# Kernel optimization log

Measured on AMD Instinct MI355X. Metric: run time of the kernel, lower is better.

The kernel has to match this reference:

```python
import jax, jax.numpy as jnp
import numpy as np

DIM = 1024
NHEAD = 16
HEAD_DIM = DIM // NHEAD


def setup_inputs() -> dict:
    key = jax.random.key(0)
    k_x, k_wqkv, k_bqkv, k_wp, k_bp = jax.random.split(key, 5)
    scale = 1.0 / np.sqrt(DIM)
    return {
        "x": jax.random.normal(k_x, (4, 2048, DIM), dtype=jnp.float32),
        "w_qkv": jax.random.uniform(k_wqkv, (DIM, 3 * DIM), minval=-scale, maxval=scale, dtype=jnp.float32),
        "b_qkv": jax.random.uniform(k_bqkv, (3 * DIM,), minval=-scale, maxval=scale, dtype=jnp.float32),
        "w_proj": jax.random.uniform(k_wp, (DIM, DIM), minval=-scale, maxval=scale, dtype=jnp.float32),
        "b_proj": jax.random.uniform(k_bp, (DIM,), minval=-scale, maxval=scale, dtype=jnp.float32),
    }


def reference(x, w_qkv, b_qkv, w_proj, b_proj):
    B, N, D = x.shape
    # qkv projection: [B,N,3D] -> [3,B,H,N,hd]
    qkv = x @ w_qkv + b_qkv
    qkv = qkv.reshape(B, N, 3, NHEAD, HEAD_DIM).transpose(2, 0, 3, 1, 4)
    q, k, v = qkv[0], qkv[1], qkv[2]
    # naive full attention: scores [B,H,N,N]
    attn = jnp.einsum("bhqd,bhkd->bhqk", q, k) / jnp.sqrt(jnp.float32(HEAD_DIM))
    attn = jax.nn.softmax(attn, axis=-1)
    out = jnp.einsum("bhqk,bhkd->bhqd", attn, v)  # [B,H,N,hd]
    out = out.transpose(0, 2, 1, 3).reshape(B, N, D)
    return out @ w_proj + b_proj
```

## Files before the change

kernel.cpp:

```cpp
#include <hip/hip_runtime.h>
#include <math.h>

#define DIM     1024
#define NHEAD   16
#define HD      64
#define BATCH   4
#define SEQ     2048
#define MTOT    (BATCH * SEQ)
#define QKV_N   (3 * DIM)

typedef __attribute__((ext_vector_type(8))) short bf16x8;
typedef __attribute__((ext_vector_type(4))) float f32x4;
typedef unsigned int u32;
typedef unsigned short u16;

__device__ __forceinline__ u16 f2bf(float f) {
    u32 u = __float_as_uint(f);
    return (u16)((u + 0x7fffu + ((u >> 16) & 1u)) >> 16);
}

__device__ __forceinline__ float exp2_fast(float x) {
    float r; asm("v_exp_f32 %0, %1" : "=v"(r) : "v"(x)); return r;
}

__device__ __forceinline__ u32 cvtpk_bf16(float lo, float hi) {
    u32 r; asm("v_cvt_pk_bf16_f32 %0, %1, %2" : "=v"(r) : "v"(lo), "v"(hi));
    return r;
}

__device__ __forceinline__ void gload_lds16(const u16* g, u16* l) {
    __builtin_amdgcn_global_load_lds((const __attribute__((address_space(1))) u32*)g,
                                     (__attribute__((address_space(3))) u32*)l, 16, 0, 0);
}

__global__ __launch_bounds__(256) void cast_x(const float* __restrict__ in,
                                              u16* __restrict__ out) {
    const int i = (blockIdx.x * 256 + threadIdx.x) * 4;
    const float4 v = *(const float4*)&in[i];
    ushort4 o;
    o.x = f2bf(v.x); o.y = f2bf(v.y); o.z = f2bf(v.z); o.w = f2bf(v.w);
    *(ushort4*)&out[i] = o;
}

__global__ __launch_bounds__(256) void cast_transpose(const float* __restrict__ W,
                                                      u16* __restrict__ Wt,
                                                      int K, int N) {
    __shared__ float Ls[64][65];
    const int k0 = blockIdx.x * 64, n0 = blockIdx.y * 64;
    const int t = threadIdx.x;
    const int r = t >> 4, c4 = (t & 15) << 2;
    #pragma unroll
    for (int i = 0; i < 4; ++i) {
        const float4 v = *(const float4*)&W[(size_t)(k0 + r + i * 16) * N + n0 + c4];
        Ls[r + i * 16][c4 + 0] = v.x; Ls[r + i * 16][c4 + 1] = v.y;
        Ls[r + i * 16][c4 + 2] = v.z; Ls[r + i * 16][c4 + 3] = v.w;
    }
    __syncthreads();
    #pragma unroll
    for (int i = 0; i < 4; ++i) {
        const int nr = r + i * 16;
        ushort4 o;
        o.x = f2bf(Ls[c4 + 0][nr]); o.y = f2bf(Ls[c4 + 1][nr]);
        o.z = f2bf(Ls[c4 + 2][nr]); o.w = f2bf(Ls[c4 + 3][nr]);
        *(ushort4*)&Wt[(size_t)(n0 + nr) * K + k0 + c4] = o;
    }
}

#define GEMM_STAGE(buf, kof, Aptr, Bptr)                                       \
    _Pragma("unroll") for (int i = 0; i < 2; ++i) {                            \
        const int row = w * 32 + i * 16 + (lane >> 2);                         \
        const int slot = (lane & 3) ^ ((row >> 1) & 3);                        \
        gload_lds16(&Aptr[(size_t)(m0 + row) * DIM + (kof) + slot * 8],        \
                    &As[buf][(w * 32 + i * 16) * 32]);                         \
        gload_lds16(&Bptr[(size_t)(n0 + row) * DIM + (kof) + slot * 8],        \
                    &Bs[buf][(w * 32 + i * 16) * 32]);                         \
    }

#define GEMM_MAINLOOP(Aptr, Bptr)                                              \
    __shared__ __align__(16) u16 As[2][128 * 32];                              \
    __shared__ __align__(16) u16 Bs[2][128 * 32];                              \
    const int t = threadIdx.x;                                                 \
    const int lane = t & 63, w = t >> 6;                                       \
    const int n0 = blockIdx.x * 128;                                           \
    const int m0 = blockIdx.y * 128;                                           \
    const int wm = (w & 1) * 64, wn = (w >> 1) * 64;                           \
    const int g = lane >> 4, li = lane & 15;                                   \
    f32x4 acc[4][4];                                                           \
    _Pragma("unroll") for (int mt = 0; mt < 4; ++mt)                           \
        _Pragma("unroll") for (int nt = 0; nt < 4; ++nt)                       \
            acc[mt][nt] = (f32x4){0.f, 0.f, 0.f, 0.f};                         \
    GEMM_STAGE(0, 0, Aptr, Bptr)                                               \
    __syncthreads();                                                           \
    int cur = 0;                                                               \
    for (int k0 = 0; k0 < DIM; k0 += 32) {                                     \
        if (k0 + 32 < DIM) { GEMM_STAGE(cur ^ 1, k0 + 32, Aptr, Bptr) }        \
        bf16x8 a[4], b[4];                                                     \
        _Pragma("unroll") for (int mt = 0; mt < 4; ++mt) {                     \
            const int row = wm + mt * 16 + li;                                 \
            const int slot = g ^ ((row >> 1) & 3);                             \
            a[mt] = *(const bf16x8*)&As[cur][row * 32 + slot * 8];             \
        }                                                                      \
        _Pragma("unroll") for (int nt = 0; nt < 4; ++nt) {                     \
            const int row = wn + nt * 16 + li;                                 \
            const int slot = g ^ ((row >> 1) & 3);                             \
            b[nt] = *(const bf16x8*)&Bs[cur][row * 32 + slot * 8];             \
        }                                                                      \
        _Pragma("unroll") for (int mt = 0; mt < 4; ++mt)                       \
            _Pragma("unroll") for (int nt = 0; nt < 4; ++nt)                   \
                acc[mt][nt] = __builtin_amdgcn_mfma_f32_16x16x32_bf16(         \
                    a[mt], b[nt], acc[mt][nt], 0, 0, 0);                       \
        __syncthreads();                                                       \
        cur ^= 1;                                                              \
    }

#define QSCALE 0.18033688011112042f
__global__ __launch_bounds__(256) void gemm_qkv(
    const u16* __restrict__ A, const u16* __restrict__ Bt,
    const float* __restrict__ bias,
    u16* __restrict__ qo, u16* __restrict__ ko, u16* __restrict__ vo)
{
    GEMM_MAINLOOP(A, Bt)
    #pragma unroll
    for (int nt = 0; nt < 4; ++nt) {
        const int n = n0 + wn + nt * 16 + li;
        const int which = n >> 10;
        const int head  = (n >> 6) & 15;
        const int hd    = n & 63;
        const float bv = bias[n];
        if (which == 2) {
            #pragma unroll
            for (int mt = 0; mt < 4; ++mt) {
                const int m = m0 + wm + mt * 16 + g * 4;
                const int bb = m >> 11, tok = m & 2047;
                const u32 p0 = cvtpk_bf16(acc[mt][nt][0] + bv, acc[mt][nt][1] + bv);
                const u32 p1 = cvtpk_bf16(acc[mt][nt][2] + bv, acc[mt][nt][3] + bv);
                u16* d = &vo[((size_t)(bb * NHEAD + head) * HD + hd) * SEQ + tok];
                *(u32*)&d[0] = p0;
                *(u32*)&d[2] = p1;
            }
        } else {
            u16* dst = (which == 0) ? qo : ko;
            const float scale = (which == 0) ? QSCALE : 1.0f;
            #pragma unroll
            for (int mt = 0; mt < 4; ++mt) {
                #pragma unroll
                for (int r = 0; r < 4; ++r) {
                    const int m = m0 + wm + mt * 16 + g * 4 + r;
                    const int bb = m >> 11, tok = m & 2047;
                    dst[((size_t)(bb * NHEAD + head) * SEQ + tok) * HD + hd] =
                        f2bf((acc[mt][nt][r] + bv) * scale);
                }
            }
        }
    }
}

__global__ __launch_bounds__(256) void gemm_proj(
    const u16* __restrict__ A, const u16* __restrict__ Bt,
    const float* __restrict__ bias, float* __restrict__ out)
{
    GEMM_MAINLOOP(A, Bt)
    #pragma unroll
    for (int nt = 0; nt < 4; ++nt) {
        const int n = n0 + wn + nt * 16 + li;
        const float bv = bias[n];
        #pragma unroll
        for (int mt = 0; mt < 4; ++mt) {
            #pragma unroll
            for (int r = 0; r < 4; ++r) {
                const int m = m0 + wm + mt * 16 + g * 4 + r;
                out[(size_t)m * DIM + n] = acc[mt][nt][r] + bv;
            }
        }
    }
}

#define NKT  (SEQ / 64)
#define ATTN_STAGE(buf, ktile)                                                 \
    _Pragma("unroll") for (int i = 0; i < 2; ++i) {                            \
        const int rho = w * 16 + i * 8 + srow;                                 \
        const int key = (rho & 32) | (((rho >> 2) & 3) << 3)                   \
                      | (((rho >> 4) & 1) << 2) | (rho & 3);                   \
        const int sl = (sslot ^ (rho & 7)) << 3;                               \
        gload_lds16(&kg[(size_t)(ktile) * (64 * HD) + (size_t)key * HD + sl],  \
                    &Ks[buf][(w * 16 + i * 8) * 64]);                          \
        gload_lds16(&vg[(size_t)rho * SEQ + (ktile) * 64 + sl],                \
                    &Vs[buf][(w * 16 + i * 8) * 64]);                          \
    }

__global__ __launch_bounds__(256) void attn_mfma(
    const u16* __restrict__ q, const u16* __restrict__ k,
    const u16* __restrict__ v, u16* __restrict__ ao)
{
    __shared__ __align__(16) u16 Ks[2][64 * 64];
    __shared__ __align__(16) u16 Vs[2][64 * 64];

    const int t = threadIdx.x;
    const int lane = t & 63, w = t >> 6;
    const int g = lane >> 4, li = lane & 15;

    int flat = blockIdx.y * 16 + blockIdx.x;
    flat = (flat & 7) * 128 + (flat >> 3);
    const int q0 = (flat & 15) * 128;
    const int bh = flat >> 4;
    const size_t base = (size_t)bh * SEQ * HD;
    const u16* kg = k + base;
    const u16* vg = v + (size_t)bh * HD * SEQ;

    bf16x8 qf[2][2];
    #pragma unroll
    for (int h = 0; h < 2; ++h) {
        const size_t qrow = base + (size_t)(q0 + w * 32 + h * 16 + li) * HD;
        qf[h][0] = *(const bf16x8*)&q[qrow + g * 8];
        qf[h][1] = *(const bf16x8*)&q[qrow + 32 + g * 8];
    }

    float lsum[2] = {0.f, 0.f};
    f32x4 oacc[2][4];
    #pragma unroll
    for (int h = 0; h < 2; ++h)
        #pragma unroll
        for (int nt = 0; nt < 4; ++nt) oacc[h][nt] = (f32x4){0.f, 0.f, 0.f, 0.f};

    const int srow = lane >> 3;
    const int sslot = lane & 7;
    const int x8 = li & 7;

    ATTN_STAGE(0, 0)
    __syncthreads();

    int cur = 0;
    for (int kt = 0; kt < NKT; ++kt) {
        if (kt + 1 < NKT) { ATTN_STAGE(cur ^ 1, kt + 1) }
        const u16* Kc = Ks[cur];
        const u16* Vc = Vs[cur];

        f32x4 s[2][4];
        #pragma unroll
        for (int nt = 0; nt < 4; ++nt) {
            const int rowb = (nt * 16 + li) << 6;
            const bf16x8 kf0 = *(const bf16x8*)&Kc[rowb + ((g ^ x8) << 3)];
            const bf16x8 kf1 = *(const bf16x8*)&Kc[rowb + (((g ^ 4) ^ x8) << 3)];
            #pragma unroll
            for (int h = 0; h < 2; ++h) {
                f32x4 c = (f32x4){0.f, 0.f, 0.f, 0.f};
                c = __builtin_amdgcn_mfma_f32_16x16x32_bf16(kf0, qf[h][0], c, 0, 0, 0);
                c = __builtin_amdgcn_mfma_f32_16x16x32_bf16(kf1, qf[h][1], c, 0, 0, 0);
                s[h][nt] = c;
            }
        }

        bf16x8 pb[2][2];
        #pragma unroll
        for (int h = 0; h < 2; ++h) {
            float rs = 0.f;
            #pragma unroll
            for (int nt = 0; nt < 4; ++nt)
                #pragma unroll
                for (int r = 0; r < 4; ++r) {
                    const float p = exp2_fast(s[h][nt][r]);
                    s[h][nt][r] = p;
                    rs += p;
                }
            lsum[h] += rs;
            #pragma unroll
            for (int ks = 0; ks < 2; ++ks) {
                union { u32 u[4]; bf16x8 v8; } uu;
                uu.u[0] = cvtpk_bf16(s[h][2 * ks][0],     s[h][2 * ks][1]);
                uu.u[1] = cvtpk_bf16(s[h][2 * ks][2],     s[h][2 * ks][3]);
                uu.u[2] = cvtpk_bf16(s[h][2 * ks + 1][0], s[h][2 * ks + 1][1]);
                uu.u[3] = cvtpk_bf16(s[h][2 * ks + 1][2], s[h][2 * ks + 1][3]);
                pb[h][ks] = uu.v8;
            }
        }

        #pragma unroll
        for (int ks = 0; ks < 2; ++ks) {
            #pragma unroll
            for (int nt = 0; nt < 4; ++nt) {
                const bf16x8 vb = *(const bf16x8*)
                    &Vc[((nt * 16 + li) << 6) + (((g ^ (ks << 2)) ^ x8) << 3)];
                #pragma unroll
                for (int h = 0; h < 2; ++h)
                    oacc[h][nt] = __builtin_amdgcn_mfma_f32_16x16x32_bf16(
                        vb, pb[h][ks], oacc[h][nt], 0, 0, 0);
            }
        }
        __syncthreads();
        cur ^= 1;
    }

    const int bb = bh >> 4, hh = bh & 15;
    #pragma unroll
    for (int h = 0; h < 2; ++h) {
        float lf = lsum[h];
        lf += __shfl_xor(lf, 16);
        lf += __shfl_xor(lf, 32);
        const float inv = 1.0f / lf;
        const int tok = q0 + w * 32 + h * 16 + li;
        u16* dst = &ao[(size_t)(bb * SEQ + tok) * DIM + hh * HD];
        #pragma unroll
        for (int nt = 0; nt < 4; ++nt) {
            const u32 p0 = cvtpk_bf16(oacc[h][nt][0] * inv, oacc[h][nt][1] * inv);
            const u32 p1 = cvtpk_bf16(oacc[h][nt][2] * inv, oacc[h][nt][3] * inv);
            *(u32*)&dst[nt * 16 + g * 4]     = p0;
            *(u32*)&dst[nt * 16 + g * 4 + 2] = p1;
        }
    }
}

extern "C" void kernel_launch(void* const* d_in, const int* in_sizes, int n_in,
                              void* d_out, int out_size, void* d_ws, size_t ws_size,
                              hipStream_t stream)
{
    const float* x      = (const float*)d_in[0];
    const float* w_qkv  = (const float*)d_in[1];
    const float* b_qkv  = (const float*)d_in[2];
    const float* w_proj = (const float*)d_in[3];
    const float* b_proj = (const float*)d_in[4];
    float* out = (float*)d_out;

    u16* xb  = (u16*)d_ws;
    u16* wqt = xb  + (size_t)MTOT * DIM;
    u16* wpt = wqt + (size_t)QKV_N * DIM;
    u16* qb  = wpt + (size_t)DIM * DIM;
    u16* kb  = qb  + (size_t)MTOT * DIM;
    u16* vb  = kb  + (size_t)MTOT * DIM;
    u16* aob = vb  + (size_t)MTOT * DIM;

    cast_x<<<(MTOT * DIM) / 1024, 256, 0, stream>>>(x, xb);
    cast_transpose<<<dim3(DIM / 64, QKV_N / 64), 256, 0, stream>>>(w_qkv, wqt, DIM, QKV_N);
    cast_transpose<<<dim3(DIM / 64, DIM / 64), 256, 0, stream>>>(w_proj, wpt, DIM, DIM);

    gemm_qkv<<<dim3(QKV_N / 128, MTOT / 128), 256, 0, stream>>>(xb, wqt, b_qkv, qb, kb, vb);
    attn_mfma<<<dim3(SEQ / 128, BATCH * NHEAD), 256, 0, stream>>>(qb, kb, vb, aob);
    gemm_proj<<<dim3(DIM / 128, MTOT / 128), 256, 0, stream>>>(aob, wpt, b_proj, out);
}
```

Measured before the change: 210.2 us.

## Double attention block to 512 threads, add MFMA priority hints, fuse prep kernels

The attention kernel now uses 8 waves per block covering 256 queries, so each K/V tile loaded into LDS is shared by twice as many query rows and each thread issues one staging load per tile instead of two. MFMA sections are wrapped in s_setprio raises so matrix work is favoured over the softmax phase of other waves. The three cast and transpose kernels are merged into one launch to cut launch overhead. The changes trade fewer blocks and possibly lower occupancy for better K/V reuse, and the block-to-work remap changes the L2 locality pattern.

```diff
diff --git a/kernel.cpp b/kernel.cpp
--- a/kernel.cpp
+++ b/kernel.cpp
@@ -33,36 +33,42 @@
                                      (__attribute__((address_space(3))) u32*)l, 16, 0, 0);
 }
 
-__global__ __launch_bounds__(256) void cast_x(const float* __restrict__ in,
-                                              u16* __restrict__ out) {
-    const int i = (blockIdx.x * 256 + threadIdx.x) * 4;
-    const float4 v = *(const float4*)&in[i];
-    ushort4 o;
-    o.x = f2bf(v.x); o.y = f2bf(v.y); o.z = f2bf(v.z); o.w = f2bf(v.w);
-    *(ushort4*)&out[i] = o;
-}
-
-__global__ __launch_bounds__(256) void cast_transpose(const float* __restrict__ W,
-                                                      u16* __restrict__ Wt,
-                                                      int K, int N) {
+__global__ __launch_bounds__(256) void prep(
+    const float* __restrict__ x,  u16* __restrict__ xb,
+    const float* __restrict__ wq, u16* __restrict__ wqt,
+    const float* __restrict__ wp, u16* __restrict__ wpt)
+{
+    const int b = blockIdx.x;
+    if (b < 8192) {
+        const int i = (b * 256 + threadIdx.x) * 4;
+        const float4 v = *(const float4*)&x[i];
+        ushort4 o;
+        o.x = f2bf(v.x); o.y = f2bf(v.y); o.z = f2bf(v.z); o.w = f2bf(v.w);
+        *(ushort4*)&xb[i] = o;
+        return;
+    }
     __shared__ float Ls[64][65];
-    const int k0 = blockIdx.x * 64, n0 = blockIdx.y * 64;
+    int i = b - 8192;
+    const float* W; u16* Wt; int N;
+    if (i < 768) { W = wq; Wt = wqt; N = QKV_N; }
+    else         { i -= 768; W = wp; Wt = wpt; N = DIM; }
+    const int k0 = (i & 15) * 64, n0 = (i >> 4) * 64;
     const int t = threadIdx.x;
     const int r = t >> 4, c4 = (t & 15) << 2;
     #pragma unroll
-    for (int i = 0; i < 4; ++i) {
-        const float4 v = *(const float4*)&W[(size_t)(k0 + r + i * 16) * N + n0 + c4];
-        Ls[r + i * 16][c4 + 0] = v.x; Ls[r + i * 16][c4 + 1] = v.y;
-        Ls[r + i * 16][c4 + 2] = v.z; Ls[r + i * 16][c4 + 3] = v.w;
+    for (int j = 0; j < 4; ++j) {
+        const float4 v = *(const float4*)&W[(size_t)(k0 + r + j * 16) * N + n0 + c4];
+        Ls[r + j * 16][c4 + 0] = v.x; Ls[r + j * 16][c4 + 1] = v.y;
+        Ls[r + j * 16][c4 + 2] = v.z; Ls[r + j * 16][c4 + 3] = v.w;
     }
     __syncthreads();
     #pragma unroll
-    for (int i = 0; i < 4; ++i) {
-        const int nr = r + i * 16;
+    for (int j = 0; j < 4; ++j) {
+        const int nr = r + j * 16;
         ushort4 o;
         o.x = f2bf(Ls[c4 + 0][nr]); o.y = f2bf(Ls[c4 + 1][nr]);
         o.z = f2bf(Ls[c4 + 2][nr]); o.w = f2bf(Ls[c4 + 3][nr]);
-        *(ushort4*)&Wt[(size_t)(n0 + nr) * K + k0 + c4] = o;
+        *(ushort4*)&Wt[(size_t)(n0 + nr) * DIM + k0 + c4] = o;
     }
 }
 
@@ -177,18 +183,14 @@
 
 #define NKT  (SEQ / 64)
 #define ATTN_STAGE(buf, ktile)                                                 \
-    _Pragma("unroll") for (int i = 0; i < 2; ++i) {                            \
-        const int rho = w * 16 + i * 8 + srow;                                 \
-        const int key = (rho & 32) | (((rho >> 2) & 3) << 3)                   \
-                      | (((rho >> 4) & 1) << 2) | (rho & 3);                   \
-        const int sl = (sslot ^ (rho & 7)) << 3;                               \
+    {                                                                          \
         gload_lds16(&kg[(size_t)(ktile) * (64 * HD) + (size_t)key * HD + sl],  \
-                    &Ks[buf][(w * 16 + i * 8) * 64]);                          \
+                    &Ks[buf][(w * 8) * 64]);                                   \
         gload_lds16(&vg[(size_t)rho * SEQ + (ktile) * 64 + sl],                \
-                    &Vs[buf][(w * 16 + i * 8) * 64]);                          \
-    }
-
-__global__ __launch_bounds__(256) void attn_mfma(
+                    &Vs[buf][(w * 8) * 64]);                                   \
+    }
+
+__global__ __launch_bounds__(512) void attn_mfma(
     const u16* __restrict__ q, const u16* __restrict__ k,
     const u16* __restrict__ v, u16* __restrict__ ao)
 {
@@ -199,10 +201,10 @@
     const int lane = t & 63, w = t >> 6;
     const int g = lane >> 4, li = lane & 15;
 
-    int flat = blockIdx.y * 16 + blockIdx.x;
-    flat = (flat & 7) * 128 + (flat >> 3);
-    const int q0 = (flat & 15) * 128;
-    const int bh = flat >> 4;
+    int flat = blockIdx.y * 8 + blockIdx.x;
+    flat = (flat & 7) * 64 + (flat >> 3);
+    const int q0 = (flat & 7) * 256;
+    const int bh = flat >> 3;
     const size_t base = (size_t)bh * SEQ * HD;
     const u16* kg = k + base;
     const u16* vg = v + (size_t)bh * HD * SEQ;
@@ -224,6 +226,10 @@
 
     const int srow = lane >> 3;
     const int sslot = lane & 7;
+    const int rho = w * 8 + srow;
+    const int key = (rho & 32) | (((rho >> 2) & 3) << 3)
+                  | (((rho >> 4) & 1) << 2) | (rho & 3);
+    const int sl = (sslot ^ (rho & 7)) << 3;
     const int x8 = li & 7;
 
     ATTN_STAGE(0, 0)
@@ -236,6 +242,7 @@
         const u16* Vc = Vs[cur];
 
         f32x4 s[2][4];
+        __builtin_amdgcn_s_setprio(1);
         #pragma unroll
         for (int nt = 0; nt < 4; ++nt) {
             const int rowb = (nt * 16 + li) << 6;
@@ -249,6 +256,7 @@
                 s[h][nt] = c;
             }
         }
+        __builtin_amdgcn_s_setprio(0);
 
         bf16x8 pb[2][2];
         #pragma unroll
@@ -274,6 +282,7 @@
             }
         }
 
+        __builtin_amdgcn_s_setprio(1);
         #pragma unroll
         for (int ks = 0; ks < 2; ++ks) {
             #pragma unroll
@@ -286,6 +295,8 @@
                         vb, pb[h][ks], oacc[h][nt], 0, 0, 0);
             }
         }
+        __builtin_amdgcn_s_setprio(0);
+
         __syncthreads();
         cur ^= 1;
     }
@@ -328,11 +339,8 @@
     u16* vb  = kb  + (size_t)MTOT * DIM;
     u16* aob = vb  + (size_t)MTOT * DIM;
 
-    cast_x<<<(MTOT * DIM) / 1024, 256, 0, stream>>>(x, xb);
-    cast_transpose<<<dim3(DIM / 64, QKV_N / 64), 256, 0, stream>>>(w_qkv, wqt, DIM, QKV_N);
-    cast_transpose<<<dim3(DIM / 64, DIM / 64), 256, 0, stream>>>(w_proj, wpt, DIM, DIM);
-
+    prep<<<8192 + 768 + 256, 256, 0, stream>>>(x, xb, w_qkv, wqt, w_proj, wpt);
     gemm_qkv<<<dim3(QKV_N / 128, MTOT / 128), 256, 0, stream>>>(xb, wqt, b_qkv, qb, kb, vb);
-    attn_mfma<<<dim3(SEQ / 128, BATCH * NHEAD), 256, 0, stream>>>(qb, kb, vb, aob);
+    attn_mfma<<<dim3(SEQ / 256, BATCH * NHEAD), 512, 0, stream>>>(qb, kb, vb, aob);
     gemm_proj<<<dim3(DIM / 128, MTOT / 128), 256, 0, stream>>>(aob, wpt, b_proj, out);
 }
```

Result: faster. 189.4 us (median of 2 runs) (-9.9%).
